# Kernel tuning notes

Hardware: AMD Instinct MI355X
Metric: run time of the kernel (lower is better)

## Reference

```python
import jax, jax.numpy as jnp
import numpy as np

B, L, IN_DIM, D, H = 4, 1024, 256, 512, 8
DH = D // H
LARGE_NEG = -10000.0
LN_EPS = 1e-5


def _layernorm(x, g, b):
    mu = jnp.mean(x, axis=-1, keepdims=True)
    var = jnp.mean((x - mu) ** 2, axis=-1, keepdims=True)
    return (x - mu) * jax.lax.rsqrt(var + LN_EPS) * g + b


def setup_inputs() -> dict:
    key = jax.random.key(0)
    ks = jax.random.split(key, 16)
    s = 0.02
    return {
        "x": jax.random.normal(ks[0], (B, L, IN_DIM), jnp.float32),
        "attention_mask": jax.random.bernoulli(ks[1], 0.5, (B, L, L)),
        "adjacency_matrix": jax.random.uniform(ks[2], (B, L, L), jnp.float32),
        "W_fuse": jax.random.normal(ks[3], (D, IN_DIM), jnp.float32) * s,
        "b_fuse": jnp.zeros((D,), jnp.float32),
        "in_proj_w": jax.random.normal(ks[4], (3 * D, D), jnp.float32) * s,
        "in_proj_b": jnp.zeros((3 * D,), jnp.float32),
        "out_w": jax.random.normal(ks[5], (D, D), jnp.float32) * s,
        "out_b": jnp.zeros((D,), jnp.float32),
        "ln1_g": jnp.ones((D,), jnp.float32),
        "ln1_b": jnp.zeros((D,), jnp.float32),
        "ln2_g": jnp.ones((D,), jnp.float32),
        "ln2_b": jnp.zeros((D,), jnp.float32),
        "W1": jax.random.normal(ks[6], (4 * D, D), jnp.float32) * s,
        "b1": jnp.zeros((4 * D,), jnp.float32),
        "W2": jax.random.normal(ks[7], (D, 4 * D), jnp.float32) * s,
        "b2": jnp.zeros((D,), jnp.float32),
        "log_scale": jnp.array(0.0, jnp.float32),  # log(adj_bias_strength=1.0)
    }


def reference(x, attention_mask, adjacency_matrix, W_fuse, b_fuse, in_proj_w,
              in_proj_b, out_w, out_b, ln1_g, ln1_b, ln2_g, ln2_b,
              W1, b1, W2, b2, log_scale):
    # fuse projection (in_dim != d_model)
    x = jnp.einsum("bli,di->bld", x, W_fuse) + b_fuse

    # ensure_self_loops_in_mask: unmask diagonal of fully-masked rows
    eye = jnp.eye(L, dtype=bool)
    row_all = jnp.all(attention_mask, axis=-1)  # [B, L]
    mask = attention_mask & ~(eye[None, :, :] & row_all[:, :, None])

    # additive attention bias: large_neg where masked + scaled clipped adjacency
    bias = jnp.where(mask, LARGE_NEG, 0.0) + \
        jnp.exp(log_scale) * jnp.clip(adjacency_matrix, 0.0, 1.0)  # [B, L, L]

    # --- attention block (pre-norm) ---
    x_norm = _layernorm(x, ln1_g, ln1_b)
    qkv = jnp.einsum("bld,ed->ble", x_norm, in_proj_w) + in_proj_b
    q, k, v = jnp.split(qkv, 3, axis=-1)
    q = q.reshape(B, L, H, DH).transpose(0, 2, 1, 3)  # [B,H,L,DH]
    k = k.reshape(B, L, H, DH).transpose(0, 2, 1, 3)
    v = v.reshape(B, L, H, DH).transpose(0, 2, 1, 3)
    scores = jnp.einsum("bhqd,bhkd->bhqk", q, k) / np.sqrt(DH) + bias[:, None]
    probs = jax.nn.softmax(scores, axis=-1)
    ctx = jnp.einsum("bhqk,bhkd->bhqd", probs, v)
    ctx = ctx.transpose(0, 2, 1, 3).reshape(B, L, D)
    attn_out = jnp.einsum("bld,ed->ble", ctx, out_w) + out_b
    x = x + attn_out

    # --- FFN block (pre-norm) ---
    x_norm = _layernorm(x, ln2_g, ln2_b)
    h = jax.nn.gelu(jnp.einsum("bld,fd->blf", x_norm, W1) + b1, approximate=False)
    ff = jnp.einsum("blf,df->bld", h, W2) + b2
    return x + ff
```

## Files before the change

kernel.cpp:

```cpp
#include <hip/hip_runtime.h>
#include <math.h>

typedef unsigned short UST;
typedef __attribute__((ext_vector_type(8))) short bf16x8;
typedef __attribute__((ext_vector_type(4))) float f32x4;

#define BB 4
#define LL 1024
#define IND 256
#define DD 512
#define HH 8
#define FFD 2048
#define NT (BB*LL)

__device__ __forceinline__ float bf2f(UST u){ return __uint_as_float(((unsigned)u)<<16); }
__device__ __forceinline__ UST f2bf(float f){
  unsigned u = __float_as_uint(f);
  u += 0x7FFFu + ((u>>16)&1u);
  return (UST)(u>>16);
}
__device__ __forceinline__ float ldF(const void* p, long i, int isf32){
  return isf32 ? ((const float*)p)[i] : bf2f(((const UST*)p)[i]);
}
__device__ __forceinline__ bool ldMask(const void* p, long i, int fm){
  if (fm==0) return ((const int*)p)[i] != 0;
  if (fm==1) return ((const unsigned char*)p)[i] != 0;
  if (fm==2) return ((const UST*)p)[i] != 0;
  return ((const float*)p)[i] != 0.f;
}
__device__ __forceinline__ f32x4 mfma16(bf16x8 a, bf16x8 b, f32x4 c){
  return __builtin_amdgcn_mfma_f32_16x16x32_bf16(a, b, c, 0, 0, 0);
}
__device__ __forceinline__ void gld16(const void* g, void* l){
  __builtin_amdgcn_global_load_lds((const __attribute__((address_space(1))) unsigned int*)g,
                                   (__attribute__((address_space(3))) unsigned int*)l, 16, 0, 0);
}

__global__ void detect_k(int* flags, const UST* xh, const unsigned int* mw){
  int lane = threadIdx.x & 63;
  int e0 = (xh[lane] >> 7) & 0xFF;
  int e1 = (xh[64+lane] >> 7) & 0xFF;
  int f32 = __any((e0 >= 140) || (e1 >= 140)) ? 1 : 0;
  unsigned v = mw[lane];
  int w01   = __all(v <= 1u) ? 1 : 0;
  unsigned lo = v & 0xFFFFu, hi = v >> 16;
  int half  = __all((lo==0u||lo==0x3F80u) && (hi==0u||hi==0x3F80u)) ? 1 : 0;
  int wordF = __all(v==0u || v==0x3F800000u) ? 1 : 0;
  int byteB = __all((v & 0xFEFEFEFEu) == 0u) ? 1 : 0;
  if (lane == 0){
    flags[0] = f32;
    flags[1] = w01 ? 0 : (half ? (wordF ? 3 : 2) : (byteB ? 1 : 0));
  }
}

struct CvtArgs { const void* src[11]; UST* dst[11]; int n[11]; };
__global__ __launch_bounds__(256) void cvt_k(const int* flags, CvtArgs a){
  int ti = blockIdx.y;
  int n = a.n[ti];
  long i8 = ((long)blockIdx.x*256 + threadIdx.x)*8;
  if (i8 >= n) return;
  const void* s = a.src[ti]; UST* d = a.dst[ti];
  if (flags[0]){
    const float4* sf = (const float4*)s;
    float4 a0 = sf[i8>>2], a1 = sf[(i8>>2)+1];
    UST o[8] = { f2bf(a0.x),f2bf(a0.y),f2bf(a0.z),f2bf(a0.w),
                 f2bf(a1.x),f2bf(a1.y),f2bf(a1.z),f2bf(a1.w) };
    *(int4*)(d+i8) = *(const int4*)o;
  } else {
    ((int4*)d)[i8>>3] = ((const int4*)s)[i8>>3];
  }
}

__global__ __launch_bounds__(256) void bias_k(const int* flags, const void* mask,
                                              const void* adj, const void* lsp, UST* biasOut){
  int fF = flags[0], fM = flags[1];
  int row = blockIdx.x;
  int i = row & (LL-1);
  long base = (long)row * LL;
  int t = threadIdx.x;
  int j0 = t*4;
  bool mv[4];
  if (fM == 0){
    int4 m4 = *(const int4*)((const int*)mask + base + j0);
    mv[0]=m4.x!=0; mv[1]=m4.y!=0; mv[2]=m4.z!=0; mv[3]=m4.w!=0;
  } else {
    #pragma unroll
    for (int k=0;k<4;++k) mv[k] = ldMask(mask, base + j0 + k, fM);
  }
  float a4[4];
  if (fF){
    float4 av = *(const float4*)((const float*)adj + base + j0);
    a4[0]=av.x; a4[1]=av.y; a4[2]=av.z; a4[3]=av.w;
  } else {
    const UST* ap = (const UST*)adj + base + j0;
    #pragma unroll
    for (int k=0;k<4;++k) a4[k] = bf2f(ap[k]);
  }
  int my = (mv[0]&&mv[1]&&mv[2]&&mv[3]) ? 1 : 0;
  int wa = __all(my);
  __shared__ int sAll[4];
  int w = t >> 6;
  if ((t & 63) == 0) sAll[w] = wa;
  __syncthreads();
  int rowAll = sAll[0] & sAll[1] & sAll[2] & sAll[3];
  float es = expf(ldF(lsp, 0, fF));
  UST o4[4];
  #pragma unroll
  for (int k = 0; k < 4; ++k){
    int j = j0 + k;
    float a = fminf(fmaxf(a4[k], 0.f), 1.f);
    bool eff = mv[k] && !((rowAll != 0) && (j == i));
    o4[k] = f2bf(((eff ? -10000.f : 0.f) + es * a) * 1.44269504f);
  }
  *(int2*)(biasOut + base + j0) = *(const int2*)o4;
}

template<int NI, int ACT, int RES, int OUTMODE>
__global__ __launch_bounds__(256) void gemm2_k(const int* flags,
    const UST* __restrict__ A, const UST* __restrict__ Bw, const UST* __restrict__ bias,
    const float* __restrict__ resid, void* Cout, int M, int N, int K){
  constexpr int TN = 32*NI;
  __shared__ UST sA[2][128*64];
  __shared__ UST sB[2][TN*64];
  int t = threadIdx.x, w = t>>6, lane = t&63, l15 = lane&15, qd = lane>>4;
  int m0 = blockIdx.x*128, n0 = blockIdx.y*TN;
  int wm = (w&1)*64, wn = (w>>1)*(NI*16);
  f32x4 acc[4][NI];
  #pragma unroll
  for (int mi=0; mi<4; ++mi)
    #pragma unroll
    for (int ni=0; ni<NI; ++ni){ acc[mi][ni][0]=0;acc[mi][ni][1]=0;acc[mi][ni][2]=0;acc[mi][ni][3]=0; }
  int sRow = lane>>3, sCol = (lane&7)*8;
  const UST* aS = A + (long)(m0 + w*32 + sRow)*K + sCol;
  const UST* bS = Bw + (long)(n0 + w*(TN/4) + sRow)*K + sCol;
  #define STAGE(buf, k0) { \
    _Pragma("unroll") \
    for (int c=0;c<4;++c) gld16(aS + (long)c*8*K + (k0), (char*)&sA[buf][(w*32 + c*8)*64]); \
    _Pragma("unroll") \
    for (int c=0;c<NI;++c) gld16(bS + (long)c*8*K + (k0), (char*)&sB[buf][(w*(TN/4) + c*8)*64]); }
  STAGE(0, 0)
  for (int k0 = 0; k0 < K; k0 += 64){
    int cur = (k0>>6)&1, nxt = cur^1;
    __syncthreads();
    if (k0 + 64 < K) STAGE(nxt, k0+64)
    #pragma unroll
    for (int ks=0; ks<2; ++ks){
      bf16x8 afr[4], bfr[NI];
      #pragma unroll
      for (int mi=0; mi<4; ++mi) afr[mi] = *(const bf16x8*)&sA[cur][(wm + mi*16 + l15)*64 + ks*32 + qd*8];
      #pragma unroll
      for (int ni=0; ni<NI; ++ni) bfr[ni] = *(const bf16x8*)&sB[cur][(wn + ni*16 + l15)*64 + ks*32 + qd*8];
      #pragma unroll
      for (int mi=0; mi<4; ++mi)
        #pragma unroll
        for (int ni=0; ni<NI; ++ni)
          acc[mi][ni] = mfma16(afr[mi], bfr[ni], acc[mi][ni]);
    }
  }
  #undef STAGE
  int outF32 = (OUTMODE==1) || (OUTMODE==2 && flags[0]);
  #pragma unroll
  for (int mi=0; mi<4; ++mi){
    #pragma unroll
    for (int ni=0; ni<NI; ++ni){
      int gc = n0 + wn + ni*16 + l15;
      float bv = bf2f(bias[gc]);
      #pragma unroll
      for (int r=0; r<4; ++r){
        int grow = m0 + wm + mi*16 + qd*4 + r;
        float c = acc[mi][ni][r] + bv;
        if (ACT) c = 0.5f*c*(1.f+erff(c*0.70710678118654752f));
        long oi = (long)grow*N + gc;
        if (RES) c += resid[oi];
        if (outF32) ((float*)Cout)[oi] = c;
        else ((UST*)Cout)[oi] = f2bf(c);
      }
    }
  }
}

__global__ __launch_bounds__(256) void ln_k(const int* flags, const float* xin,
    const void* gp, const void* bp, UST* xout){
  int fF = flags[0];
  int row = blockIdx.x, t = threadIdx.x;
  const float* xr = xin + (long)row * DD;
  float v0 = xr[t], v1 = xr[t+256];
  float s = v0+v1, q = v0*v0 + v1*v1;
  #pragma unroll
  for (int off=1; off<64; off<<=1){ s += __shfl_xor(s,off,64); q += __shfl_xor(q,off,64); }
  __shared__ float rs[4], rq[4];
  int w = t>>6;
  if ((t&63)==0){ rs[w]=s; rq[w]=q; }
  __syncthreads();
  float S = rs[0]+rs[1]+rs[2]+rs[3];
  float Q = rq[0]+rq[1]+rq[2]+rq[3];
  float mean = S * (1.f/DD);
  float var  = fmaxf(Q * (1.f/DD) - mean*mean, 0.f);
  float ri = rsqrtf(var + 1e-5f);
  float g0 = ldF(gp, t, fF), b0 = ldF(bp, t, fF);
  float g1 = ldF(gp, t+256, fF), b1 = ldF(bp, t+256, fF);
  xout[(long)row*DD + t]     = f2bf((v0-mean)*ri*g0 + b0);
  xout[(long)row*DD + t+256] = f2bf((v1-mean)*ri*g1 + b1);
}

__global__ __launch_bounds__(256) void repack_v(const UST* __restrict__ qkv, UST* __restrict__ vT){
  int id = blockIdx.x;
  int bh = id & 31, qt = id >> 5;
  int b = bh >> 3, h = bh & 7;
  int t = threadIdx.x, w = t >> 6, lane = t & 63;
  int token = qt*64 + lane;
  const UST* src = qkv + ((long)(b*LL + token))*1536 + 1024 + h*64;
  #pragma unroll
  for (int c = 0; c < 2; ++c){
    int ch = w*2 + c;
    union { int4 v; UST u[8]; } uu;
    uu.v = *(const int4*)(src + ch*8);
    #pragma unroll
    for (int i = 0; i < 8; ++i)
      vT[((long)(bh*64 + ch*8 + i))*LL + token] = uu.u[i];
  }
}

__global__ __launch_bounds__(256) void attn_k(const UST* __restrict__ qkv,
    const UST* __restrict__ vT, const UST* __restrict__ bias, UST* __restrict__ ctx){
  int id = blockIdx.x;
  int b = id & 3, h = (id>>2) & 7, qt = id >> 5;
  int bh = b*HH + h;
  int q0 = qt*64;
  int t = threadIdx.x, w = t>>6, lane = t&63, l15 = lane&15, qd = lane>>4;
  __shared__ UST sK[2][2][64*32];
  __shared__ UST sV[2][2][64*32];
  __shared__ UST sB[2][2][64*32];
  __shared__ UST sP[4][16*72];
  UST* myP = &sP[w][0];

  const UST* qrow = qkv + ((long)(b*LL + q0 + w*16 + l15))*1536 + h*64;
  bf16x8 qf0 = *(const bf16x8*)(qrow + qd*8);
  bf16x8 qf1 = *(const bf16x8*)(qrow + 32 + qd*8);

  int rowS = t>>2, colS = (t&3)*8;
  const UST* kS = qkv + (long)(b*LL + rowS)*1536 + 512 + h*64 + colS;
  const UST* vS = vT + (long)(bh*64 + rowS)*LL + colS;
  const UST* bS = bias + ((long)b<<20) + (long)(q0 + rowS)*LL + colS;

  f32x4 o[4]; float lsum[4];
  #pragma unroll
  for (int i=0;i<4;i++){ o[i][0]=0;o[i][1]=0;o[i][2]=0;o[i][3]=0; lsum[i]=0.f; }
  const float C1 = 0.18033688f;

  gld16(kS,      (char*)sK[0][0] + w*1024);
  gld16(kS + 32, (char*)sK[0][1] + w*1024);
  gld16(vS,      (char*)sV[0][0] + w*1024);
  gld16(vS + 32, (char*)sV[0][1] + w*1024);
  gld16(bS,      (char*)sB[0][0] + w*1024);
  gld16(bS + 32, (char*)sB[0][1] + w*1024);

  for (int kt = 0; kt < 16; ++kt){
    int cur = kt&1, nxt = cur^1;
    int k0 = kt*64;
    __syncthreads();
    if (kt < 15){
      int kn = k0 + 64;
      gld16(kS + (long)kn*1536,      (char*)sK[nxt][0] + w*1024);
      gld16(kS + (long)kn*1536 + 32, (char*)sK[nxt][1] + w*1024);
      gld16(vS + kn,                 (char*)sV[nxt][0] + w*1024);
      gld16(vS + kn + 32,            (char*)sV[nxt][1] + w*1024);
      gld16(bS + kn,                 (char*)sB[nxt][0] + w*1024);
      gld16(bS + kn + 32,            (char*)sB[nxt][1] + w*1024);
    }
    f32x4 s4[4];
    #pragma unroll
    for (int i=0;i<4;i++){ s4[i][0]=0;s4[i][1]=0;s4[i][2]=0;s4[i][3]=0; }
    #pragma unroll
    for (int ni=0; ni<4; ++ni){
      bf16x8 kf0 = *(const bf16x8*)&sK[cur][0][(ni*16+l15)*32 + qd*8];
      bf16x8 kf1 = *(const bf16x8*)&sK[cur][1][(ni*16+l15)*32 + qd*8];
      s4[ni] = mfma16(qf0, kf0, s4[ni]);
      s4[ni] = mfma16(qf1, kf1, s4[ni]);
    }
    float p[4][4];
    #pragma unroll
    for (int ni=0; ni<4; ++ni){
      const UST* sBc = sB[cur][ni>>1];
      int nc = (ni & 1)*16 + l15;
      #pragma unroll
      for (int r=0; r<4; ++r){
        float bzv = bf2f(sBc[(w*16 + qd*4 + r)*32 + nc]);
        p[ni][r] = exp2f(fmaf(s4[ni][r], C1, bzv));
      }
    }
    #pragma unroll
    for (int r=0; r<4; ++r)
      lsum[r] += (p[0][r]+p[1][r]) + (p[2][r]+p[3][r]);
    #pragma unroll
    for (int ni=0; ni<4; ++ni)
      #pragma unroll
      for (int r=0; r<4; ++r) myP[(qd*4+r)*72 + ni*16 + l15] = f2bf(p[ni][r]);
    bf16x8 pf0 = *(const bf16x8*)&myP[l15*72 + qd*8];
    bf16x8 pf1 = *(const bf16x8*)&myP[l15*72 + 32 + qd*8];
    #pragma unroll
    for (int dn=0; dn<4; ++dn){
      bf16x8 vf0 = *(const bf16x8*)&sV[cur][0][(dn*16+l15)*32 + qd*8];
      bf16x8 vf1 = *(const bf16x8*)&sV[cur][1][(dn*16+l15)*32 + qd*8];
      o[dn] = mfma16(pf0, vf0, o[dn]);
      o[dn] = mfma16(pf1, vf1, o[dn]);
    }
  }
  float linv[4];
  #pragma unroll
  for (int r=0; r<4; ++r){
    float s = lsum[r];
    #pragma unroll
    for (int off=1; off<16; off<<=1) s += __shfl_xor(s, off, 64);
    linv[r] = 1.f / s;
  }
  #pragma unroll
  for (int dn=0; dn<4; ++dn){
    #pragma unroll
    for (int r=0; r<4; ++r){
      long oi = ((long)(b*LL + q0 + w*16 + qd*4 + r))*DD + h*64 + dn*16 + l15;
      ctx[oi] = f2bf(o[dn][r] * linv[r]);
    }
  }
}

extern "C" void kernel_launch(void* const* d_in, const int* in_sizes, int n_in,
                              void* d_out, int out_size, void* d_ws, size_t ws_size,
                              hipStream_t stream){
  char* ws = (char*)d_ws;
  size_t o = 0;
  auto alloc = [&](size_t b){ size_t r = o; o += (b + 255) & ~(size_t)255; return r; };
  int*   flags = (int*)(ws + alloc(256));
  size_t biasOff = alloc(8UL<<20);
  size_t qkvOff  = alloc(12UL<<20);
  UST* biasC = (UST*)(ws + biasOff);
  UST* qkv   = (UST*)(ws + qkvOff);
  UST* hb    = (UST*)(ws + biasOff);
  UST* vT    = (UST*)(ws + alloc(4UL<<20));
  UST* xbf   = (UST*)(ws + alloc(2UL<<20));
  UST* wfuse = (UST*)(ws + alloc(131072*2));
  UST* bfuse = (UST*)(ws + alloc(1024));
  UST* ipw   = (UST*)(ws + alloc(786432*2));
  UST* ipb   = (UST*)(ws + alloc(3072*2));
  UST* outw  = (UST*)(ws + alloc(262144*2));
  UST* outb  = (UST*)(ws + alloc(1024));
  UST* w1    = (UST*)(ws + alloc(1048576*2));
  UST* b1    = (UST*)(ws + alloc(4096*2));
  UST* w2    = (UST*)(ws + alloc(1048576*2));
  UST* b2    = (UST*)(ws + alloc(1024));
  float* xf  = (float*)(ws + alloc((size_t)NT*DD*4));
  UST* xn    = (UST*)(ws + alloc((size_t)NT*DD*2));
  UST* ctx   = (UST*)(ws + alloc((size_t)NT*DD*2));
  float* x2  = (float*)(ws + alloc((size_t)NT*DD*4));

  detect_k<<<1, 64, 0, stream>>>(flags, (const UST*)d_in[0], (const unsigned int*)d_in[1]);

  CvtArgs ca;
  const int srcIdx[11] = {0,3,4,5,6,7,8,13,14,15,16};
  UST* dsts[11] = {xbf,wfuse,bfuse,ipw,ipb,outw,outb,w1,b1,w2,b2};
  const int ns[11] = {NT*IND, DD*IND, DD, 3*DD*DD, 3*DD, DD*DD, DD, FFD*DD, FFD, DD*FFD, DD};
  for (int i=0;i<11;i++){ ca.src[i]=d_in[srcIdx[i]]; ca.dst[i]=dsts[i]; ca.n[i]=ns[i]; }
  cvt_k<<<dim3(512,11), 256, 0, stream>>>(flags, ca);

  bias_k<<<BB*LL, 256, 0, stream>>>(flags, d_in[1], d_in[2], d_in[17], biasC);

  gemm2_k<2,0,0,1><<<dim3(32,8), 256, 0, stream>>>(flags, xbf, wfuse, bfuse, nullptr, xf, NT, DD, IND);
  ln_k<<<NT, 256, 0, stream>>>(flags, xf, d_in[9], d_in[10], xn);
  gemm2_k<4,0,0,0><<<dim3(32,12), 256, 0, stream>>>(flags, xn, ipw, ipb, nullptr, qkv, NT, 3*DD, DD);
  repack_v<<<512, 256, 0, stream>>>(qkv, vT);
  attn_k<<<512, 256, 0, stream>>>(qkv, vT, biasC, ctx);
  gemm2_k<2,0,1,1><<<dim3(32,8), 256, 0, stream>>>(flags, ctx, outw, outb, xf, x2, NT, DD, DD);
  ln_k<<<NT, 256, 0, stream>>>(flags, x2, d_in[11], d_in[12], xn);
  gemm2_k<4,1,0,0><<<dim3(32,16), 256, 0, stream>>>(flags, xn, w1, b1, nullptr, hb, NT, FFD, DD);
  gemm2_k<2,0,1,2><<<dim3(32,8), 256, 0, stream>>>(flags, hb, w2, b2, x2, d_out, NT, DD, FFD);
}
```

Measured before the change: 262.9 us.

## Merge prep kernels, retile GEMMs to 64-row tiles, swizzle LDS layouts

Merges the bf16 conversion kernel and the attention-bias kernel into one launch with a block-index split. Replaces the GEMM with a templated TM/TN version using 64-row tiles, which doubles the block count on the grid. The GEMM and attention kernels also change their LDS layouts so each lane loads 8 contiguous rows in column-major chunks, meant to reduce shared-memory bank conflicts on fragment reads. Smaller tiles give more blocks to fill the GPU but lower the data reuse per block.

```diff
diff --git a/kernel.cpp b/kernel.cpp
--- a/kernel.cpp
+++ b/kernel.cpp
@@ -54,113 +54,121 @@
 }
 
 struct CvtArgs { const void* src[11]; UST* dst[11]; int n[11]; };
-__global__ __launch_bounds__(256) void cvt_k(const int* flags, CvtArgs a){
-  int ti = blockIdx.y;
-  int n = a.n[ti];
-  long i8 = ((long)blockIdx.x*256 + threadIdx.x)*8;
-  if (i8 >= n) return;
-  const void* s = a.src[ti]; UST* d = a.dst[ti];
-  if (flags[0]){
-    const float4* sf = (const float4*)s;
-    float4 a0 = sf[i8>>2], a1 = sf[(i8>>2)+1];
-    UST o[8] = { f2bf(a0.x),f2bf(a0.y),f2bf(a0.z),f2bf(a0.w),
-                 f2bf(a1.x),f2bf(a1.y),f2bf(a1.z),f2bf(a1.w) };
-    *(int4*)(d+i8) = *(const int4*)o;
+__global__ __launch_bounds__(256) void prep_k(const int* flags, CvtArgs a,
+    const void* mask, const void* adj, const void* lsp, UST* biasOut){
+  int bid = blockIdx.x;
+  int t = threadIdx.x;
+  if (bid < BB*LL){
+    int fF = flags[0], fM = flags[1];
+    int row = bid;
+    int i = row & (LL-1);
+    long base = (long)row * LL;
+    int j0 = t*4;
+    bool mv[4];
+    if (fM == 0){
+      int4 m4 = *(const int4*)((const int*)mask + base + j0);
+      mv[0]=m4.x!=0; mv[1]=m4.y!=0; mv[2]=m4.z!=0; mv[3]=m4.w!=0;
+    } else {
+      #pragma unroll
+      for (int k=0;k<4;++k) mv[k] = ldMask(mask, base + j0 + k, fM);
+    }
+    float a4[4];
+    if (fF){
+      float4 av = *(const float4*)((const float*)adj + base + j0);
+      a4[0]=av.x; a4[1]=av.y; a4[2]=av.z; a4[3]=av.w;
+    } else {
+      const UST* ap = (const UST*)adj + base + j0;
+      #pragma unroll
+      for (int k=0;k<4;++k) a4[k] = bf2f(ap[k]);
+    }
+    int my = (mv[0]&&mv[1]&&mv[2]&&mv[3]) ? 1 : 0;
+    int wa = __all(my);
+    __shared__ int sAll[4];
+    int w = t >> 6;
+    if ((t & 63) == 0) sAll[w] = wa;
+    __syncthreads();
+    int rowAll = sAll[0] & sAll[1] & sAll[2] & sAll[3];
+    float es = expf(ldF(lsp, 0, fF));
+    UST o4[4];
+    #pragma unroll
+    for (int k = 0; k < 4; ++k){
+      int j = j0 + k;
+      float av = fminf(fmaxf(a4[k], 0.f), 1.f);
+      bool eff = mv[k] && !((rowAll != 0) && (j == i));
+      o4[k] = f2bf(((eff ? -10000.f : 0.f) + es * av) * 1.44269504f);
+    }
+    *(int2*)(biasOut + base + j0) = *(const int2*)o4;
   } else {
-    ((int4*)d)[i8>>3] = ((const int4*)s)[i8>>3];
-  }
-}
-
-__global__ __launch_bounds__(256) void bias_k(const int* flags, const void* mask,
-                                              const void* adj, const void* lsp, UST* biasOut){
-  int fF = flags[0], fM = flags[1];
-  int row = blockIdx.x;
-  int i = row & (LL-1);
-  long base = (long)row * LL;
-  int t = threadIdx.x;
-  int j0 = t*4;
-  bool mv[4];
-  if (fM == 0){
-    int4 m4 = *(const int4*)((const int*)mask + base + j0);
-    mv[0]=m4.x!=0; mv[1]=m4.y!=0; mv[2]=m4.z!=0; mv[3]=m4.w!=0;
-  } else {
-    #pragma unroll
-    for (int k=0;k<4;++k) mv[k] = ldMask(mask, base + j0 + k, fM);
-  }
-  float a4[4];
-  if (fF){
-    float4 av = *(const float4*)((const float*)adj + base + j0);
-    a4[0]=av.x; a4[1]=av.y; a4[2]=av.z; a4[3]=av.w;
-  } else {
-    const UST* ap = (const UST*)adj + base + j0;
-    #pragma unroll
-    for (int k=0;k<4;++k) a4[k] = bf2f(ap[k]);
-  }
-  int my = (mv[0]&&mv[1]&&mv[2]&&mv[3]) ? 1 : 0;
-  int wa = __all(my);
-  __shared__ int sAll[4];
-  int w = t >> 6;
-  if ((t & 63) == 0) sAll[w] = wa;
-  __syncthreads();
-  int rowAll = sAll[0] & sAll[1] & sAll[2] & sAll[3];
-  float es = expf(ldF(lsp, 0, fF));
-  UST o4[4];
-  #pragma unroll
-  for (int k = 0; k < 4; ++k){
-    int j = j0 + k;
-    float a = fminf(fmaxf(a4[k], 0.f), 1.f);
-    bool eff = mv[k] && !((rowAll != 0) && (j == i));
-    o4[k] = f2bf(((eff ? -10000.f : 0.f) + es * a) * 1.44269504f);
-  }
-  *(int2*)(biasOut + base + j0) = *(const int2*)o4;
-}
-
-template<int NI, int ACT, int RES, int OUTMODE>
-__global__ __launch_bounds__(256) void gemm2_k(const int* flags,
+    int cb = bid - BB*LL;
+    int ti = cb >> 9, xi = cb & 511;
+    int n = a.n[ti];
+    long i8 = ((long)xi*256 + t)*8;
+    if (i8 >= n) return;
+    const void* s = a.src[ti]; UST* d = a.dst[ti];
+    if (flags[0]){
+      const float4* sf = (const float4*)s;
+      float4 a0 = sf[i8>>2], a1 = sf[(i8>>2)+1];
+      UST o[8] = { f2bf(a0.x),f2bf(a0.y),f2bf(a0.z),f2bf(a0.w),
+                   f2bf(a1.x),f2bf(a1.y),f2bf(a1.z),f2bf(a1.w) };
+      *(int4*)(d+i8) = *(const int4*)o;
+    } else {
+      ((int4*)d)[i8>>3] = ((const int4*)s)[i8>>3];
+    }
+  }
+}
+
+template<int TM, int TN, int ACT, int RES, int OUTMODE>
+__global__ __launch_bounds__(256) void gemm3_k(const int* flags,
     const UST* __restrict__ A, const UST* __restrict__ Bw, const UST* __restrict__ bias,
     const float* __restrict__ resid, void* Cout, int M, int N, int K){
-  constexpr int TN = 32*NI;
-  __shared__ UST sA[2][128*64];
+  constexpr int MI = TM/32, NI = TN/32;
+  __shared__ UST sA[2][TM*64];
   __shared__ UST sB[2][TN*64];
   int t = threadIdx.x, w = t>>6, lane = t&63, l15 = lane&15, qd = lane>>4;
-  int m0 = blockIdx.x*128, n0 = blockIdx.y*TN;
-  int wm = (w&1)*64, wn = (w>>1)*(NI*16);
-  f32x4 acc[4][NI];
-  #pragma unroll
-  for (int mi=0; mi<4; ++mi)
+  int m0 = blockIdx.x*TM, n0 = blockIdx.y*TN;
+  int wm = (w&1)*(TM/2), wn = (w>>1)*(TN/2);
+  f32x4 acc[MI][NI];
+  #pragma unroll
+  for (int mi=0; mi<MI; ++mi)
     #pragma unroll
     for (int ni=0; ni<NI; ++ni){ acc[mi][ni][0]=0;acc[mi][ni][1]=0;acc[mi][ni][2]=0;acc[mi][ni][3]=0; }
-  int sRow = lane>>3, sCol = (lane&7)*8;
-  const UST* aS = A + (long)(m0 + w*32 + sRow)*K + sCol;
+  int sRow = lane&7, sCol = (lane>>3)*8;
+  const UST* aS = A + (long)(m0 + w*(TM/4) + sRow)*K + sCol;
   const UST* bS = Bw + (long)(n0 + w*(TN/4) + sRow)*K + sCol;
-  #define STAGE(buf, k0) { \
-    _Pragma("unroll") \
-    for (int c=0;c<4;++c) gld16(aS + (long)c*8*K + (k0), (char*)&sA[buf][(w*32 + c*8)*64]); \
-    _Pragma("unroll") \
-    for (int c=0;c<NI;++c) gld16(bS + (long)c*8*K + (k0), (char*)&sB[buf][(w*(TN/4) + c*8)*64]); }
-  STAGE(0, 0)
+  auto stage = [&](int buf, int k0){
+    #pragma unroll
+    for (int c=0;c<MI;++c) gld16(aS + (long)c*8*K + k0, (char*)&sA[buf][(w*(TM/4)+c*8)*64]);
+    #pragma unroll
+    for (int c=0;c<NI;++c) gld16(bS + (long)c*8*K + k0, (char*)&sB[buf][(w*(TN/4)+c*8)*64]);
+  };
+  stage(0, 0);
   for (int k0 = 0; k0 < K; k0 += 64){
     int cur = (k0>>6)&1, nxt = cur^1;
     __syncthreads();
-    if (k0 + 64 < K) STAGE(nxt, k0+64)
+    if (k0 + 64 < K) stage(nxt, k0+64);
     #pragma unroll
     for (int ks=0; ks<2; ++ks){
-      bf16x8 afr[4], bfr[NI];
-      #pragma unroll
-      for (int mi=0; mi<4; ++mi) afr[mi] = *(const bf16x8*)&sA[cur][(wm + mi*16 + l15)*64 + ks*32 + qd*8];
-      #pragma unroll
-      for (int ni=0; ni<NI; ++ni) bfr[ni] = *(const bf16x8*)&sB[cur][(wn + ni*16 + l15)*64 + ks*32 + qd*8];
-      #pragma unroll
-      for (int mi=0; mi<4; ++mi)
+      bf16x8 afr[MI], bfr[NI];
+      #pragma unroll
+      for (int mi=0; mi<MI; ++mi){
+        int R = wm + mi*16 + l15;
+        afr[mi] = *(const bf16x8*)&sA[cur][(R>>3)*512 + (ks*4+qd)*64 + (R&7)*8];
+      }
+      #pragma unroll
+      for (int ni=0; ni<NI; ++ni){
+        int R = wn + ni*16 + l15;
+        bfr[ni] = *(const bf16x8*)&sB[cur][(R>>3)*512 + (ks*4+qd)*64 + (R&7)*8];
+      }
+      #pragma unroll
+      for (int mi=0; mi<MI; ++mi)
         #pragma unroll
         for (int ni=0; ni<NI; ++ni)
           acc[mi][ni] = mfma16(afr[mi], bfr[ni], acc[mi][ni]);
     }
   }
-  #undef STAGE
   int outF32 = (OUTMODE==1) || (OUTMODE==2 && flags[0]);
   #pragma unroll
-  for (int mi=0; mi<4; ++mi){
+  for (int mi=0; mi<MI; ++mi){
     #pragma unroll
     for (int ni=0; ni<NI; ++ni){
       int gc = n0 + wn + ni*16 + l15;
@@ -238,9 +246,9 @@
   bf16x8 qf0 = *(const bf16x8*)(qrow + qd*8);
   bf16x8 qf1 = *(const bf16x8*)(qrow + 32 + qd*8);
 
+  const UST* kS = qkv + (long)(b*LL + w*16 + (lane&15))*1536 + 512 + h*64 + (lane>>4)*8;
+  const UST* vS = vT + (long)(bh*64 + w*16 + (lane&15))*LL + (lane>>4)*8;
   int rowS = t>>2, colS = (t&3)*8;
-  const UST* kS = qkv + (long)(b*LL + rowS)*1536 + 512 + h*64 + colS;
-  const UST* vS = vT + (long)(bh*64 + rowS)*LL + colS;
   const UST* bS = bias + ((long)b<<20) + (long)(q0 + rowS)*LL + colS;
 
   f32x4 o[4]; float lsum[4];
@@ -248,33 +256,28 @@
   for (int i=0;i<4;i++){ o[i][0]=0;o[i][1]=0;o[i][2]=0;o[i][3]=0; lsum[i]=0.f; }
   const float C1 = 0.18033688f;
 
-  gld16(kS,      (char*)sK[0][0] + w*1024);
-  gld16(kS + 32, (char*)sK[0][1] + w*1024);
-  gld16(vS,      (char*)sV[0][0] + w*1024);
-  gld16(vS + 32, (char*)sV[0][1] + w*1024);
-  gld16(bS,      (char*)sB[0][0] + w*1024);
-  gld16(bS + 32, (char*)sB[0][1] + w*1024);
+  auto stage = [&](int buf, int k0){
+    gld16(kS + (long)k0*1536,      (char*)sK[buf][0] + w*1024);
+    gld16(kS + (long)k0*1536 + 32, (char*)sK[buf][1] + w*1024);
+    gld16(vS + k0,                 (char*)sV[buf][0] + w*1024);
+    gld16(vS + k0 + 32,            (char*)sV[buf][1] + w*1024);
+    gld16(bS + k0,                 (char*)sB[buf][0] + w*1024);
+    gld16(bS + k0 + 32,            (char*)sB[buf][1] + w*1024);
+  };
+  stage(0, 0);
 
   for (int kt = 0; kt < 16; ++kt){
     int cur = kt&1, nxt = cur^1;
     int k0 = kt*64;
     __syncthreads();
-    if (kt < 15){
-      int kn = k0 + 64;
-      gld16(kS + (long)kn*1536,      (char*)sK[nxt][0] + w*1024);
-      gld16(kS + (long)kn*1536 + 32, (char*)sK[nxt][1] + w*1024);
-      gld16(vS + kn,                 (char*)sV[nxt][0] + w*1024);
-      gld16(vS + kn + 32,            (char*)sV[nxt][1] + w*1024);
-      gld16(bS + kn,                 (char*)sB[nxt][0] + w*1024);
-      gld16(bS + kn + 32,            (char*)sB[nxt][1] + w*1024);
-    }
+    if (kt < 15) stage(nxt, k0+64);
     f32x4 s4[4];
     #pragma unroll
     for (int i=0;i<4;i++){ s4[i][0]=0;s4[i][1]=0;s4[i][2]=0;s4[i][3]=0; }
     #pragma unroll
     for (int ni=0; ni<4; ++ni){
-      bf16x8 kf0 = *(const bf16x8*)&sK[cur][0][(ni*16+l15)*32 + qd*8];
-      bf16x8 kf1 = *(const bf16x8*)&sK[cur][1][(ni*16+l15)*32 + qd*8];
+      bf16x8 kf0 = *(const bf16x8*)&sK[cur][0][ni*512 + qd*128 + l15*8];
+      bf16x8 kf1 = *(const bf16x8*)&sK[cur][1][ni*512 + qd*128 + l15*8];
       s4[ni] = mfma16(qf0, kf0, s4[ni]);
       s4[ni] = mfma16(qf1, kf1, s4[ni]);
     }
@@ -300,8 +303,8 @@
     bf16x8 pf1 = *(const bf16x8*)&myP[l15*72 + 32 + qd*8];
     #pragma unroll
     for (int dn=0; dn<4; ++dn){
-      bf16x8 vf0 = *(const bf16x8*)&sV[cur][0][(dn*16+l15)*32 + qd*8];
-      bf16x8 vf1 = *(const bf16x8*)&sV[cur][1][(dn*16+l15)*32 + qd*8];
+      bf16x8 vf0 = *(const bf16x8*)&sV[cur][0][dn*512 + qd*128 + l15*8];
+      bf16x8 vf1 = *(const bf16x8*)&sV[cur][1][dn*512 + qd*128 + l15*8];
       o[dn] = mfma16(pf0, vf0, o[dn]);
       o[dn] = mfma16(pf1, vf1, o[dn]);
     }
@@ -360,17 +363,15 @@
   UST* dsts[11] = {xbf,wfuse,bfuse,ipw,ipb,outw,outb,w1,b1,w2,b2};
   const int ns[11] = {NT*IND, DD*IND, DD, 3*DD*DD, 3*DD, DD*DD, DD, FFD*DD, FFD, DD*FFD, DD};
   for (int i=0;i<11;i++){ ca.src[i]=d_in[srcIdx[i]]; ca.dst[i]=dsts[i]; ca.n[i]=ns[i]; }
-  cvt_k<<<dim3(512,11), 256, 0, stream>>>(flags, ca);
-
-  bias_k<<<BB*LL, 256, 0, stream>>>(flags, d_in[1], d_in[2], d_in[17], biasC);
-
-  gemm2_k<2,0,0,1><<<dim3(32,8), 256, 0, stream>>>(flags, xbf, wfuse, bfuse, nullptr, xf, NT, DD, IND);
+  prep_k<<<BB*LL + 11*512, 256, 0, stream>>>(flags, ca, d_in[1], d_in[2], d_in[17], biasC);
+
+  gemm3_k<64,64,0,0,1><<<dim3(64,8), 256, 0, stream>>>(flags, xbf, wfuse, bfuse, nullptr, xf, NT, DD, IND);
   ln_k<<<NT, 256, 0, stream>>>(flags, xf, d_in[9], d_in[10], xn);
-  gemm2_k<4,0,0,0><<<dim3(32,12), 256, 0, stream>>>(flags, xn, ipw, ipb, nullptr, qkv, NT, 3*DD, DD);
+  gemm3_k<64,128,0,0,0><<<dim3(64,12), 256, 0, stream>>>(flags, xn, ipw, ipb, nullptr, qkv, NT, 3*DD, DD);
   repack_v<<<512, 256, 0, stream>>>(qkv, vT);
   attn_k<<<512, 256, 0, stream>>>(qkv, vT, biasC, ctx);
-  gemm2_k<2,0,1,1><<<dim3(32,8), 256, 0, stream>>>(flags, ctx, outw, outb, xf, x2, NT, DD, DD);
+  gemm3_k<64,64,0,1,1><<<dim3(64,8), 256, 0, stream>>>(flags, ctx, outw, outb, xf, x2, NT, DD, DD);
   ln_k<<<NT, 256, 0, stream>>>(flags, x2, d_in[11], d_in[12], xn);
-  gemm2_k<4,1,0,0><<<dim3(32,16), 256, 0, stream>>>(flags, xn, w1, b1, nullptr, hb, NT, FFD, DD);
-  gemm2_k<2,0,1,2><<<dim3(32,8), 256, 0, stream>>>(flags, hb, w2, b2, x2, d_out, NT, DD, FFD);
-}
+  gemm3_k<64,128,1,0,0><<<dim3(64,16), 256, 0, stream>>>(flags, xn, w1, b1, nullptr, hb, NT, FFD, DD);
+  gemm3_k<64,64,0,1,2><<<dim3(64,8), 256, 0, stream>>>(flags, hb, w2, b2, x2, d_out, NT, DD, FFD);
+}
```

After: 279.6 us. 6.4% more time.
